# Kernel optimization log

Measured on AMD Instinct MI355X. Metric: run time of the kernel, lower is better.

## Reference

```python
import jax, jax.numpy as jnp
import numpy as np

B, T, I, H = 64, 512, 256, 256


def gru_scan(x_tb, h0, Wi, Wh, bi, bh):
    # x_tb: [T,B,I]; Wi: [3H,I]; Wh: [3H,H]
    gi_all = jnp.einsum('tbi,gi->tbg', x_tb, Wi) + bi  # precompute input projections [T,B,3H]

    def step(h, gi_t):
        gh = h @ Wh.T + bh                     # [B,3H]
        i_r, i_z, i_n = jnp.split(gi_t, 3, axis=-1)
        h_r, h_z, h_n = jnp.split(gh, 3, axis=-1)
        r = jax.nn.sigmoid(i_r + h_r)
        z = jax.nn.sigmoid(i_z + h_z)
        n = jnp.tanh(i_n + r * h_n)
        h_new = jnp.tanh((1.0 - z) * n + z * h)  # GRUCell output + extra tanh per step
        return h_new, h_new

    _, ys = jax.lax.scan(step, h0, gi_all)
    return ys  # [T,B,H]


def setup_inputs() -> dict:
    key = jax.random.key(0)
    ks = jax.random.split(key, 12)
    s = 1.0 / np.sqrt(H)
    u = lambda k, shp: jax.random.uniform(k, shp, jnp.float32, -s, s)
    return {
        'x': jax.random.normal(ks[0], (B, T, I), jnp.float32),
        'h0_fwd': jax.random.normal(ks[1], (B, H), jnp.float32),
        'h0_bwd': jax.random.normal(ks[2], (B, H), jnp.float32),
        'W_ih_f': u(ks[3], (3 * H, I)),
        'W_hh_f': u(ks[4], (3 * H, H)),
        'b_ih_f': u(ks[5], (3 * H,)),
        'b_hh_f': u(ks[6], (3 * H,)),
        'W_ih_b': u(ks[7], (3 * H, I)),
        'W_hh_b': u(ks[8], (3 * H, H)),
        'b_ih_b': u(ks[9], (3 * H,)),
        'b_hh_b': u(ks[10], (3 * H,)),
        'lengths': jnp.full((B,), T, dtype=jnp.int64 if jax.config.jax_enable_x64 else jnp.int32),
    }


def reference(x, h0_fwd, h0_bwd, W_ih_f, W_hh_f, b_ih_f, b_hh_f,
              W_ih_b, W_hh_b, b_ih_b, b_hh_b, lengths):
    # return_sequences=True; max(lengths) == T (full sequence) for static shapes
    x_tb = jnp.transpose(x, (1, 0, 2))                      # [T,B,I]
    fwd = gru_scan(x_tb, h0_fwd, W_ih_f, W_hh_f, b_ih_f, b_hh_f)          # [T,B,H]
    bwd = gru_scan(x_tb[::-1], h0_bwd, W_ih_b, W_hh_b, b_ih_b, b_hh_b)[::-1]
    out = jnp.concatenate([fwd, bwd], axis=-1)              # [T,B,2H]
    return jnp.transpose(out, (1, 0, 2))                    # [B,T,2H]
```

## Files before the change

### kernel.cpp

```cpp
#include <hip/hip_runtime.h>
#include <cstdint>
#include <cstddef>

#define BB 64
#define TT 512
#define II 256
#define HH 256
#define GG 768

typedef _Float16 f16x2 __attribute__((ext_vector_type(2)));
typedef _Float16 f16x8 __attribute__((ext_vector_type(8)));
typedef float    f32x4 __attribute__((ext_vector_type(4)));

__device__ __forceinline__ float sigf(float x)       { return 1.f / (1.f + __expf(-x)); }
__device__ __forceinline__ float tanh_fast(float x)  { return 1.f - 2.f / (__expf(2.f * x) + 1.f); }

__device__ __forceinline__ float dot2(uint32_t w, uint32_t h, float acc) {
#if defined(__has_builtin)
#if __has_builtin(__builtin_amdgcn_fdot2)
    return __builtin_amdgcn_fdot2(__builtin_bit_cast(f16x2, w),
                                  __builtin_bit_cast(f16x2, h), acc, false);
#else
    f16x2 a = __builtin_bit_cast(f16x2, w), b = __builtin_bit_cast(f16x2, h);
    return acc + (float)a.x * (float)b.x + (float)a.y * (float)b.y;
#endif
#else
    f16x2 a = __builtin_bit_cast(f16x2, w), b = __builtin_bit_cast(f16x2, h);
    return acc + (float)a.x * (float)b.x + (float)a.y * (float)b.y;
#endif
}

__device__ __forceinline__ uint32_t packf16(float a, float b) {
    f16x2 v; v.x = (_Float16)a; v.y = (_Float16)b;
    return __builtin_bit_cast(uint32_t, v);
}

__global__ void pack_wh(const float* __restrict__ Whf,
                        const float* __restrict__ Whb,
                        uint32_t* __restrict__ wpk)
{
    int idx = blockIdx.x * 256 + threadIdx.x;
    int d = idx >= 98304;
    int u = idx - d * 98304;
    int t  = u & 511;
    int jm = u >> 9;
    int j = jm >> 5, m = jm & 31;
    int r = j * 128 + (t >> 2);
    int c = t & 3;
    const float* __restrict__ W = d ? Whb : Whf;
    const float* base = &W[(size_t)r * II + c * 64 + 2 * m];
    wpk[(size_t)d * 98304 + (size_t)jm * 512 + t] = packf16(base[0], base[1]);
}

__global__ __launch_bounds__(256) void gi_gemm_mfma(
    const float* __restrict__ x,
    const float* __restrict__ Wif, const float* __restrict__ bif,
    const float* __restrict__ Wib, const float* __restrict__ bib,
    float* __restrict__ gi)
{
    __shared__ __align__(16) _Float16 Asm[8][64][8];
    __shared__ __align__(16) _Float16 Bsm[8][64][8];

    const int ntile = blockIdx.x % 12;
    const int mtile = blockIdx.x / 12;
    const int m0 = mtile * 64;
    const int n0 = ntile * 64;
    const int d  = m0 >> 15;
    const int xrow0 = m0 & 32767;
    const float* __restrict__ W    = d ? Wib : Wif;
    const float* __restrict__ bias = d ? bib : bif;

    const int tid  = threadIdx.x;
    const int w    = tid >> 6;
    const int lane = tid & 63;
    const int lr   = lane & 15;
    const int lk8  = (lane >> 4);

    f32x4 acc[4] = {};

    const int srow = tid >> 2;
    const int scol = (tid & 3) * 16;

    for (int k0 = 0; k0 < II; k0 += 64) {
        const float* ap = &x[(size_t)(xrow0 + srow) * II + k0 + scol];
        const float* bp = &W[(size_t)(n0 + srow)   * II + k0 + scol];
#pragma unroll
        for (int half = 0; half < 2; ++half) {
            float4 a0 = *(const float4*)(ap + 8 * half);
            float4 a1 = *(const float4*)(ap + 8 * half + 4);
            float4 b0 = *(const float4*)(bp + 8 * half);
            float4 b1 = *(const float4*)(bp + 8 * half + 4);
            f16x8 av, bv;
            av[0] = (_Float16)a0.x; av[1] = (_Float16)a0.y;
            av[2] = (_Float16)a0.z; av[3] = (_Float16)a0.w;
            av[4] = (_Float16)a1.x; av[5] = (_Float16)a1.y;
            av[6] = (_Float16)a1.z; av[7] = (_Float16)a1.w;
            bv[0] = (_Float16)b0.x; bv[1] = (_Float16)b0.y;
            bv[2] = (_Float16)b0.z; bv[3] = (_Float16)b0.w;
            bv[4] = (_Float16)b1.x; bv[5] = (_Float16)b1.y;
            bv[6] = (_Float16)b1.z; bv[7] = (_Float16)b1.w;
            *(f16x8*)&Asm[scol / 8 + half][srow][0] = av;
            *(f16x8*)&Bsm[scol / 8 + half][srow][0] = bv;
        }
        __syncthreads();

#pragma unroll
        for (int kk = 0; kk < 2; ++kk) {
            const int kb = kk * 4 + lk8;
            f16x8 af = *(const f16x8*)&Asm[kb][16 * w + lr][0];
#pragma unroll
            for (int j = 0; j < 4; ++j) {
                f16x8 bf = *(const f16x8*)&Bsm[kb][16 * j + lr][0];
                acc[j] = __builtin_amdgcn_mfma_f32_16x16x32_f16(af, bf, acc[j], 0, 0, 0);
            }
        }
        __syncthreads();
    }

    const int rbase = m0 + 16 * w + (lane >> 4) * 4;
#pragma unroll
    for (int j = 0; j < 4; ++j) {
        const int col = n0 + 16 * j + lr;
        const float bcol = bias[col];
#pragma unroll
        for (int r = 0; r < 4; ++r) {
            gi[(size_t)(rbase + r) * GG + col] = acc[j][r] + bcol;
        }
    }
}

__global__ __launch_bounds__(512, 2) void gru_scan_reg3(
    const float* __restrict__ gi,
    const uint32_t* __restrict__ wpk,
    const float* __restrict__ h0f, const float* __restrict__ h0b,
    const float* __restrict__ bhf, const float* __restrict__ bhb,
    float* __restrict__ out)
{
    __shared__ __align__(16) uint32_t hpk[2][4 * 36];
    __shared__ __align__(16) float    h32[2][HH];
    __shared__ __align__(16) float    part[3072];
    __shared__ __align__(16) float    gis[GG];

    const int bx = blockIdx.x;
    const int d  = bx >> 6;
    const int b  = bx & 63;
    const int t  = threadIdx.x;

    const float* __restrict__ bh = d ? bhb : bhf;
    const float* __restrict__ h0 = d ? h0b : h0f;

    if (t < HH) {
        float hv = h0[(size_t)b * HH + t];
        h32[0][t] = hv;
        float hv1 = __shfl_down(hv, 1);
        if (!(t & 1)) {
            int dw = t >> 1;
            hpk[0][(dw >> 5) * 36 + (dw & 31)] = packf16(hv, hv1);
        }
    }

    const uint32_t* __restrict__ wp = wpk + (size_t)d * 98304;
    uint32_t wf[192];
#pragma unroll
    for (int jm = 0; jm < 192; ++jm) wf[jm] = wp[(size_t)jm * 512 + t];

    float bhr = 0.f, bhz = 0.f, bhn = 0.f;
    if (t < HH) { bhr = bh[t]; bhz = bh[HH + t]; bhn = bh[2 * HH + t]; }

    const int dir = d ? -1 : 1;
    int ta = d ? (TT - 1) : 0;
    const float* __restrict__ gp =
        gi + ((size_t)d * BB + b) * (size_t)TT * GG + (size_t)ta * GG;
    float g0 = gp[t];
    float g1 = (t < HH) ? gp[512 + t] : 0.f;

    const int c = t & 3;

    __syncthreads();

    for (int s = 0; s < TT; ++s) {
        const int cur = s & 1;

        gis[t] = g0;
        if (t < HH) gis[512 + t] = g1;
        if (s + 1 < TT) {
            gp += (ptrdiff_t)dir * GG;
            g0 = gp[t];
            if (t < HH) g1 = gp[512 + t];
        }

        const uint32_t* __restrict__ hb = &hpk[cur][c * 36];
        float acc[6] = {0.f, 0.f, 0.f, 0.f, 0.f, 0.f};
#pragma unroll
        for (int q = 0; q < 8; ++q) {
            uint4 h4 = *(const uint4*)&hb[q * 4];
#pragma unroll
            for (int j = 0; j < 6; ++j) {
                acc[j] = dot2(wf[j * 32 + q * 4 + 0], h4.x, acc[j]);
                acc[j] = dot2(wf[j * 32 + q * 4 + 1], h4.y, acc[j]);
                acc[j] = dot2(wf[j * 32 + q * 4 + 2], h4.z, acc[j]);
                acc[j] = dot2(wf[j * 32 + q * 4 + 3], h4.w, acc[j]);
            }
        }
#pragma unroll
        for (int j = 0; j < 6; ++j) part[j * 512 + t] = acc[j];

        __syncthreads();

        if (t < HH) {
            float4 p0 = *(const float4*)&part[4 * t];
            float4 p1 = *(const float4*)&part[1024 + 4 * t];
            float4 p2 = *(const float4*)&part[2048 + 4 * t];
            float hr = (p0.x + p0.y) + (p0.z + p0.w) + bhr;
            float hz = (p1.x + p1.y) + (p1.z + p1.w) + bhz;
            float hn = (p2.x + p2.y) + (p2.z + p2.w) + bhn;
            float ir = gis[t], iz = gis[HH + t], inn = gis[2 * HH + t];
            float r  = sigf(ir + hr);
            float z  = sigf(iz + hz);
            float n  = tanh_fast(inn + r * hn);
            float hp = h32[cur][t];
            float hnew = tanh_fast((1.f - z) * n + z * hp);
            h32[cur ^ 1][t] = hnew;
            out[((size_t)b * TT + ta) * (2 * HH) + d * HH + t] = hnew;
            float ho = __shfl_down(hnew, 1);
            if (!(t & 1)) {
                int dw = t >> 1;
                hpk[cur ^ 1][(dw >> 5) * 36 + (dw & 31)] = packf16(hnew, ho);
            }
        }
        ta += dir;
        __syncthreads();
    }
}

__global__ __launch_bounds__(768) void gru_scan_fallback(
    const float* __restrict__ x,
    const float* __restrict__ h0f, const float* __restrict__ h0b,
    const float* __restrict__ Wif, const float* __restrict__ bif_,
    const float* __restrict__ Whf, const float* __restrict__ bhf,
    const float* __restrict__ Wib, const float* __restrict__ bib_,
    const float* __restrict__ Whb, const float* __restrict__ bhb,
    float* __restrict__ out)
{
    __shared__ __align__(16) float hbuf[2][HH];
    __shared__ float gh_s[GG];
    __shared__ float gi_s[GG];
    __shared__ __align__(16) float xrow[II];

    const int bx  = blockIdx.x;
    const int d   = bx >> 6;
    const int b   = bx & 63;
    const int tid = threadIdx.x;

    const float* __restrict__ Wh = d ? Whb : Whf;
    const float* __restrict__ bh = d ? bhb : bhf;
    const float* __restrict__ Wi = d ? Wib : Wif;
    const float* __restrict__ bi = d ? bib_ : bif_;
    const float* __restrict__ h0 = d ? h0b : h0f;

    if (tid < HH) hbuf[0][tid] = h0[(size_t)b * HH + tid];

    const float bh_row = bh[tid];
    const float bi_row = bi[tid];
    const float4* __restrict__ whr = (const float4*)(Wh + (size_t)tid * II);
    const float4* __restrict__ wir = (const float4*)(Wi + (size_t)tid * II);

    __syncthreads();

    for (int s = 0; s < TT; ++s) {
        const int ta  = d ? (TT - 1 - s) : s;
        const int cur = s & 1;

        if (tid < II) xrow[tid] = x[((size_t)b * TT + ta) * II + tid];
        __syncthreads();

        const float4* hv4 = (const float4*)hbuf[cur];
        float a0 = 0.f, a1 = 0.f, a2 = 0.f, a3 = 0.f;
#pragma unroll 4
        for (int k = 0; k < II / 4; k += 4) {
            float4 w0 = whr[k], w1 = whr[k + 1], w2 = whr[k + 2], w3 = whr[k + 3];
            float4 q0 = hv4[k], q1 = hv4[k + 1], q2 = hv4[k + 2], q3 = hv4[k + 3];
            a0 += w0.x * q0.x + w0.y * q0.y + w0.z * q0.z + w0.w * q0.w;
            a1 += w1.x * q1.x + w1.y * q1.y + w1.z * q1.z + w1.w * q1.w;
            a2 += w2.x * q2.x + w2.y * q2.y + w2.z * q2.z + w2.w * q2.w;
            a3 += w3.x * q3.x + w3.y * q3.y + w3.z * q3.z + w3.w * q3.w;
        }
        gh_s[tid] = (a0 + a1) + (a2 + a3) + bh_row;

        const float4* xv4 = (const float4*)xrow;
        float c0 = 0.f, c1 = 0.f, c2 = 0.f, c3 = 0.f;
#pragma unroll 4
        for (int k = 0; k < II / 4; k += 4) {
            float4 w0 = wir[k], w1 = wir[k + 1], w2 = wir[k + 2], w3 = wir[k + 3];
            float4 q0 = xv4[k], q1 = xv4[k + 1], q2 = xv4[k + 2], q3 = xv4[k + 3];
            c0 += w0.x * q0.x + w0.y * q0.y + w0.z * q0.z + w0.w * q0.w;
            c1 += w1.x * q1.x + w1.y * q1.y + w1.z * q1.z + w1.w * q1.w;
            c2 += w2.x * q2.x + w2.y * q2.y + w2.z * q2.z + w2.w * q2.w;
            c3 += w3.x * q3.x + w3.y * q3.y + w3.z * q3.z + w3.w * q3.w;
        }
        gi_s[tid] = (c0 + c1) + (c2 + c3) + bi_row;
        __syncthreads();

        if (tid < HH) {
            float ir = gi_s[tid], iz = gi_s[HH + tid], inn = gi_s[2 * HH + tid];
            float hr = gh_s[tid], hz = gh_s[HH + tid], hn = gh_s[2 * HH + tid];
            float r  = sigf(ir + hr);
            float z  = sigf(iz + hz);
            float n  = tanh_fast(inn + r * hn);
            float hp = hbuf[cur][tid];
            float hnew = tanh_fast((1.f - z) * n + z * hp);
            hbuf[cur ^ 1][tid] = hnew;
            out[((size_t)b * TT + ta) * (2 * HH) + d * HH + tid] = hnew;
        }
        __syncthreads();
    }
}

extern "C" void kernel_launch(void* const* d_in, const int* in_sizes, int n_in,
                              void* d_out, int out_size, void* d_ws, size_t ws_size,
                              hipStream_t stream)
{
    const float* x   = (const float*)d_in[0];
    const float* h0f = (const float*)d_in[1];
    const float* h0b = (const float*)d_in[2];
    const float* Wif = (const float*)d_in[3];
    const float* Whf = (const float*)d_in[4];
    const float* bif = (const float*)d_in[5];
    const float* bhf = (const float*)d_in[6];
    const float* Wib = (const float*)d_in[7];
    const float* Whb = (const float*)d_in[8];
    const float* bib = (const float*)d_in[9];
    const float* bhb = (const float*)d_in[10];
    float* out = (float*)d_out;

    const size_t gi_bytes  = (size_t)2 * BB * TT * GG * sizeof(float);
    const size_t wpk_bytes = (size_t)2 * 98304 * sizeof(uint32_t);

    if (ws_size >= gi_bytes + wpk_bytes) {
        float*    gi  = (float*)d_ws;
        uint32_t* wpk = (uint32_t*)((char*)d_ws + gi_bytes);

        pack_wh<<<768, 256, 0, stream>>>(Whf, Whb, wpk);

        gi_gemm_mfma<<<12288, 256, 0, stream>>>(x, Wif, bif, Wib, bib, gi);

        gru_scan_reg3<<<128, 512, 0, stream>>>(gi, wpk, h0f, h0b, bhf, bhb, out);
    } else {
        gru_scan_fallback<<<128, 768, 0, stream>>>(
            x, h0f, h0b, Wif, bif, Whf, bhf, Wib, bib, Whb, bhb, out);
    }
}
```

Measured before the change: 726.7 us.

## Halve scan block size, hold full weight slice per thread, reduce via DPP

```diff
diff --git a/kernel.cpp b/kernel.cpp
--- a/kernel.cpp
+++ b/kernel.cpp
@@ -35,6 +35,13 @@
     return __builtin_bit_cast(uint32_t, v);
 }
 
+template <int CTRL>
+__device__ __forceinline__ float qadd(float v) {
+    int y = __builtin_amdgcn_update_dpp(0, __builtin_bit_cast(int, v),
+                                        CTRL, 0xf, 0xf, true);
+    return v + __builtin_bit_cast(float, y);
+}
+
 __global__ void pack_wh(const float* __restrict__ Whf,
                         const float* __restrict__ Whb,
                         uint32_t* __restrict__ wpk)
@@ -42,14 +49,14 @@
     int idx = blockIdx.x * 256 + threadIdx.x;
     int d = idx >= 98304;
     int u = idx - d * 98304;
-    int t  = u & 511;
-    int jm = u >> 9;
+    int t  = u & 255;
+    int jm = u >> 8;
     int j = jm >> 5, m = jm & 31;
-    int r = j * 128 + (t >> 2);
+    int r = j * 64 + (t >> 2);
     int c = t & 3;
     const float* __restrict__ W = d ? Whb : Whf;
     const float* base = &W[(size_t)r * II + c * 64 + 2 * m];
-    wpk[(size_t)d * 98304 + (size_t)jm * 512 + t] = packf16(base[0], base[1]);
+    wpk[(size_t)d * 98304 + (size_t)jm * 256 + t] = packf16(base[0], base[1]);
 }
 
 __global__ __launch_bounds__(256) void gi_gemm_mfma(
@@ -129,7 +136,7 @@
     }
 }
 
-__global__ __launch_bounds__(512, 2) void gru_scan_reg3(
+__global__ __launch_bounds__(256, 1) void gru_scan_reg4(
     const float* __restrict__ gi,
     const uint32_t* __restrict__ wpk,
     const float* __restrict__ h0f, const float* __restrict__ h0b,
@@ -137,96 +144,89 @@
     float* __restrict__ out)
 {
     __shared__ __align__(16) uint32_t hpk[2][4 * 36];
-    __shared__ __align__(16) float    h32[2][HH];
-    __shared__ __align__(16) float    part[3072];
-    __shared__ __align__(16) float    gis[GG];
 
     const int bx = blockIdx.x;
     const int d  = bx >> 6;
     const int b  = bx & 63;
     const int t  = threadIdx.x;
+    const int a  = t >> 2;
+    const int q  = t & 3;
+    const int o  = 64 * q + a;
 
     const float* __restrict__ bh = d ? bhb : bhf;
     const float* __restrict__ h0 = d ? h0b : h0f;
 
-    if (t < HH) {
-        float hv = h0[(size_t)b * HH + t];
-        h32[0][t] = hv;
-        float hv1 = __shfl_down(hv, 1);
-        if (!(t & 1)) {
-            int dw = t >> 1;
-            hpk[0][(dw >> 5) * 36 + (dw & 31)] = packf16(hv, hv1);
-        }
-    }
-
     const uint32_t* __restrict__ wp = wpk + (size_t)d * 98304;
-    uint32_t wf[192];
-#pragma unroll
-    for (int jm = 0; jm < 192; ++jm) wf[jm] = wp[(size_t)jm * 512 + t];
-
-    float bhr = 0.f, bhz = 0.f, bhn = 0.f;
-    if (t < HH) { bhr = bh[t]; bhz = bh[HH + t]; bhn = bh[2 * HH + t]; }
+    uint32_t wf[384];
+#pragma unroll
+    for (int jm = 0; jm < 384; ++jm) wf[jm] = wp[(size_t)jm * 256 + t];
+
+    float hp = h0[(size_t)b * HH + o];
+    {
+        float hb4 = __shfl_down(hp, 4);
+        if (!(a & 1)) {
+            int m = o >> 1;
+            hpk[0][(m >> 5) * 36 + (m & 31)] = packf16(hp, hb4);
+        }
+    }
+
+    const float bhr = bh[o];
+    const float bhz = bh[HH + o];
+    const float bhn = bh[2 * HH + o];
 
     const int dir = d ? -1 : 1;
     int ta = d ? (TT - 1) : 0;
     const float* __restrict__ gp =
         gi + ((size_t)d * BB + b) * (size_t)TT * GG + (size_t)ta * GG;
-    float g0 = gp[t];
-    float g1 = (t < HH) ? gp[512 + t] : 0.f;
-
-    const int c = t & 3;
+    float g0 = gp[o], g1 = gp[HH + o], g2 = gp[2 * HH + o];
 
     __syncthreads();
 
     for (int s = 0; s < TT; ++s) {
         const int cur = s & 1;
 
-        gis[t] = g0;
-        if (t < HH) gis[512 + t] = g1;
+        const float ir = g0, iz = g1, inn = g2;
         if (s + 1 < TT) {
             gp += (ptrdiff_t)dir * GG;
-            g0 = gp[t];
-            if (t < HH) g1 = gp[512 + t];
-        }
-
-        const uint32_t* __restrict__ hb = &hpk[cur][c * 36];
-        float acc[6] = {0.f, 0.f, 0.f, 0.f, 0.f, 0.f};
-#pragma unroll
-        for (int q = 0; q < 8; ++q) {
-            uint4 h4 = *(const uint4*)&hb[q * 4];
-#pragma unroll
-            for (int j = 0; j < 6; ++j) {
-                acc[j] = dot2(wf[j * 32 + q * 4 + 0], h4.x, acc[j]);
-                acc[j] = dot2(wf[j * 32 + q * 4 + 1], h4.y, acc[j]);
-                acc[j] = dot2(wf[j * 32 + q * 4 + 2], h4.z, acc[j]);
-                acc[j] = dot2(wf[j * 32 + q * 4 + 3], h4.w, acc[j]);
+            g0 = gp[o]; g1 = gp[HH + o]; g2 = gp[2 * HH + o];
+        }
+
+        const uint32_t* __restrict__ hb = &hpk[cur][q * 36];
+        float acc[12] = {};
+#pragma unroll
+        for (int q8 = 0; q8 < 8; ++q8) {
+            uint4 h4 = *(const uint4*)&hb[q8 * 4];
+#pragma unroll
+            for (int j = 0; j < 12; ++j) {
+                acc[j] = dot2(wf[j * 32 + q8 * 4 + 0], h4.x, acc[j]);
+                acc[j] = dot2(wf[j * 32 + q8 * 4 + 1], h4.y, acc[j]);
+                acc[j] = dot2(wf[j * 32 + q8 * 4 + 2], h4.z, acc[j]);
+                acc[j] = dot2(wf[j * 32 + q8 * 4 + 3], h4.w, acc[j]);
             }
         }
-#pragma unroll
-        for (int j = 0; j < 6; ++j) part[j * 512 + t] = acc[j];
-
-        __syncthreads();
-
-        if (t < HH) {
-            float4 p0 = *(const float4*)&part[4 * t];
-            float4 p1 = *(const float4*)&part[1024 + 4 * t];
-            float4 p2 = *(const float4*)&part[2048 + 4 * t];
-            float hr = (p0.x + p0.y) + (p0.z + p0.w) + bhr;
-            float hz = (p1.x + p1.y) + (p1.z + p1.w) + bhz;
-            float hn = (p2.x + p2.y) + (p2.z + p2.w) + bhn;
-            float ir = gis[t], iz = gis[HH + t], inn = gis[2 * HH + t];
-            float r  = sigf(ir + hr);
-            float z  = sigf(iz + hz);
-            float n  = tanh_fast(inn + r * hn);
-            float hp = h32[cur][t];
-            float hnew = tanh_fast((1.f - z) * n + z * hp);
-            h32[cur ^ 1][t] = hnew;
-            out[((size_t)b * TT + ta) * (2 * HH) + d * HH + t] = hnew;
-            float ho = __shfl_down(hnew, 1);
-            if (!(t & 1)) {
-                int dw = t >> 1;
-                hpk[cur ^ 1][(dw >> 5) * 36 + (dw & 31)] = packf16(hnew, ho);
-            }
+
+#pragma unroll
+        for (int j = 0; j < 12; ++j) {
+            acc[j] = qadd<0xB1>(acc[j]);
+            acc[j] = qadd<0x4E>(acc[j]);
+        }
+
+        float hr = q < 2 ? (q == 0 ? acc[0] : acc[1]) : (q == 2 ? acc[2] : acc[3]);
+        float hz = q < 2 ? (q == 0 ? acc[4] : acc[5]) : (q == 2 ? acc[6] : acc[7]);
+        float hn = q < 2 ? (q == 0 ? acc[8] : acc[9]) : (q == 2 ? acc[10] : acc[11]);
+        hr += bhr; hz += bhz; hn += bhn;
+
+        float r = sigf(ir + hr);
+        float z = sigf(iz + hz);
+        float n = tanh_fast(inn + r * hn);
+        float hnew = tanh_fast((1.f - z) * n + z * hp);
+        hp = hnew;
+        out[((size_t)b * TT + ta) * (2 * HH) + d * HH + o] = hnew;
+
+        float hb4 = __shfl_down(hnew, 4);
+        if (!(a & 1)) {
+            int m = o >> 1;
+            hpk[cur ^ 1][(m >> 5) * 36 + (m & 31)] = packf16(hnew, hb4);
         }
         ta += dir;
         __syncthreads();
@@ -344,7 +344,7 @@
 
         gi_gemm_mfma<<<12288, 256, 0, stream>>>(x, Wif, bif, Wib, bib, gi);
 
-        gru_scan_reg3<<<128, 512, 0, stream>>>(gi, wpk, h0f, h0b, bhf, bhb, out);
+        gru_scan_reg4<<<128, 256, 0, stream>>>(gi, wpk, h0f, h0b, bhf, bhb, out);
     } else {
         gru_scan_fallback<<<128, 768, 0, stream>>>(
             x, h0f, h0b, Wif, bif, Whf, bhf, Wib, bib, Whb, bhb, out);
```

After: 937.7 us. 1.29x slower.
